# Performance work log

Hardware: AMD Instinct MI355X
Metric: run time of the kernel (lower is better)

Reference implementation:

```python
import jax, jax.numpy as jnp
import numpy as np

H = 4        # num_heads
KNN = 10     # k_knn neighbors gathered by distance
KS = 4       # k_select top-k neighbors kept by attention score
EPS = 1e-5
BIG = 1e9


def _ln(x, g, b):
    m = x.mean(-1, keepdims=True)
    v = ((x - m) ** 2).mean(-1, keepdims=True)
    return (x - m) * jax.lax.rsqrt(v + EPS) * g + b


def _sparse_dyn_voxel_attn(x, coords, mask, w_qkv, b_qkv, w_proj, b_proj):
    # x: [B,N,C], coords: [B,N,3], mask: [B,N] bool
    B, N, C = x.shape
    dh = C // H
    qkv = x @ w_qkv + b_qkv                       # [B,N,3C]
    q, k, v = jnp.split(qkv, 3, axis=-1)
    q = q.reshape(B, N, H, dh).transpose(0, 2, 1, 3)   # [B,H,N,dh]
    k = k.reshape(B, N, H, dh).transpose(0, 2, 1, 3)
    v = v.reshape(B, N, H, dh).transpose(0, 2, 1, 3)

    # KNN over voxel coordinates; empty voxels pushed to far distance
    d2 = jnp.sum((coords[:, :, None, :] - coords[:, None, :, :]) ** 2, axis=-1)  # [B,N,N]
    d2 = jnp.where(mask[:, None, :], d2, BIG)
    _, nbr = jax.lax.top_k(-d2, KNN)              # [B,N,KNN] nearest-neighbor indices

    # gather neighbor keys/values: [B,H,N,KNN,dh]
    kn = jax.vmap(lambda a, i: a[:, i, :])(k, nbr)
    vn = jax.vmap(lambda a, i: a[:, i, :])(v, nbr)
    nmask = jax.vmap(lambda m, i: m[i])(mask, nbr)  # [B,N,KNN]

    scale = float(1.0 / np.sqrt(dh))
    scores = jnp.einsum('bhnd,bhnkd->bhnk', q, kn) * scale  # [B,H,N,KNN]
    scores = scores + jnp.where(nmask, 0.0, -BIG)[:, None, :, :]

    # dynamic selection: keep top k_select neighbors by score, softmax over them
    sv, si = jax.lax.top_k(scores, KS)            # [B,H,N,KS]
    w = jax.nn.softmax(sv, axis=-1)
    vsel = jnp.take_along_axis(vn, si[..., None], axis=3)   # [B,H,N,KS,dh]
    o = jnp.einsum('bhnk,bhnkd->bhnd', w, vsel)   # [B,H,N,dh]
    o = o.transpose(0, 2, 1, 3).reshape(B, N, C) @ w_proj + b_proj
    return jnp.where(mask[..., None], o, 0.0)


def setup_inputs() -> dict:
    key = jax.random.key(0)
    ks = jax.random.split(key, 8)
    B, N, C, M = 4, 4096, 64, 256  # N = 16^3 voxels
    s = lambda k, sh: jax.random.normal(k, sh, jnp.float32) * 0.02
    return dict(
        inputs=jax.random.normal(ks[0], (B, N, C), jnp.float32),
        voxel_coords=jax.random.uniform(ks[1], (B, N, 3), jnp.float32) * 16.0,
        non_empty_mask=jax.random.randint(ks[2], (B, N), 0, 2).astype(bool),
        ln1_g=jnp.ones(C, jnp.float32), ln1_b=jnp.zeros(C, jnp.float32),
        ln2_g=jnp.ones(C, jnp.float32), ln2_b=jnp.zeros(C, jnp.float32),
        w_qkv=s(ks[3], (C, 3 * C)), b_qkv=jnp.zeros(3 * C, jnp.float32),
        w_proj=s(ks[4], (C, C)), b_proj=jnp.zeros(C, jnp.float32),
        w1=s(ks[5], (C, M)), b1=jnp.zeros(M, jnp.float32),
        w2=s(ks[6], (M, C)), b2=jnp.zeros(C, jnp.float32),
    )


def reference(inputs, voxel_coords, non_empty_mask, ln1_g, ln1_b, ln2_g, ln2_b,
              w_qkv, b_qkv, w_proj, b_proj, w1, b1, w2, b2):
    a = _sparse_dyn_voxel_attn(_ln(inputs, ln1_g, ln1_b), voxel_coords,
                               non_empty_mask, w_qkv, b_qkv, w_proj, b_proj)
    x = 0.5 * a + inputs                          # drop_path(attn)*0.5 + shortcut (eval)
    h = jax.nn.gelu(_ln(x, ln2_g, ln2_b) @ w1 + b1) @ w2 + b2
    return 0.5 * h + x
```

## Files before the change

kernel.cpp:

```cpp
#include <hip/hip_runtime.h>
#include <hip/hip_bf16.h>
#include <math.h>

#define NH   4
#define DH   16
#define CH   64
#define KNN  10
#define KS   4
#define NV   4096
#define NB   4
#define MHID 256
#define BN   (NB * NV)

#define P_LN1G  0
#define P_LN1B  64
#define P_LN2G  128
#define P_LN2B  192
#define P_WQKV  256
#define P_BQKV  12544
#define P_WPROJ 12736
#define P_BPROJ 16832
#define P_W1    16896
#define P_B1    33280
#define P_W2    33536
#define P_B2    49920
#define P_TOT   49984

#define N_ING  (BN * CH + P_TOT + BN)
#define N_ING4 (N_ING / 4)
#define N_PACK (16384 + 16384 + 12288)
#define NPREP  ((N_ING4 + N_PACK + 255) / 256)
#define KNNBLK (NB * (NV / 4))

typedef __hip_bfloat16 bf16;
typedef __attribute__((ext_vector_type(8))) short short8;
typedef __attribute__((ext_vector_type(4))) float float4a;

__device__ __forceinline__ float b2f(bf16 x) { return __bfloat162float(x); }

__device__ __forceinline__ float cvt(const void* p, int i, int isbf) {
  return isbf ? b2f(((const bf16*)p)[i]) : ((const float*)p)[i];
}

__device__ __forceinline__ float us2f(unsigned short u) {
  return __uint_as_float(((unsigned)u) << 16);
}

__device__ __forceinline__ float4 cvt4(const void* p, int i, int isbf) {
  float4 r;
  if (isbf) {
    ushort4 u = *(const ushort4*)((const unsigned short*)p + i);
    r.x = us2f(u.x); r.y = us2f(u.y); r.z = us2f(u.z); r.w = us2f(u.w);
  } else {
    r = *(const float4*)((const float*)p + i);
  }
  return r;
}

__device__ __forceinline__ float wave_sum_f32(float v) {
#pragma unroll
  for (int m = 32; m >= 1; m >>= 1) v += __shfl_xor(v, m, 64);
  return v;
}

__device__ __forceinline__ int wave_sum_i32(int v) {
#pragma unroll
  for (int m = 32; m >= 1; m >>= 1) v += __shfl_xor(v, m, 64);
  return v;
}

__device__ __forceinline__ void wave_min_kv(unsigned& hi, unsigned& lo) {
#pragma unroll
  for (int m = 32; m >= 1; m >>= 1) {
    unsigned ohi = __shfl_xor(hi, m, 64);
    unsigned olo = __shfl_xor(lo, m, 64);
    if (ohi < hi || (ohi == hi && olo < lo)) { hi = ohi; lo = olo; }
  }
}

__device__ __forceinline__ float tanh_fast(float u) {
  float e = __expf(2.0f * u);
  return 1.0f - 2.0f / (e + 1.0f);
}

__device__ __forceinline__ float d2f(float x, float y, float z,
                                     float qx, float qy, float qz) {
  float dx = x - qx, dy = y - qy, dz = z - qz;
  return dx * dx + dy * dy + dz * dz;
}

__device__ __forceinline__ void knn_insert(unsigned long long* arr,
                                           unsigned long long key) {
  if (key < arr[KNN - 1]) {
#pragma unroll
    for (int t = 0; t < KNN; ++t) {
      unsigned long long a = arr[t];
      bool lt = key < a;
      unsigned long long mn = lt ? key : a;
      unsigned long long mx = lt ? a : key;
      arr[t] = mn;
      key = mx;
    }
  }
}

__global__ __launch_bounds__(256) void k_prep(
    const void* xin, const void* coords, const void* maskr,
    const void* ln1g, const void* ln1b, const void* ln2g, const void* ln2b,
    const void* wqkv, const void* bqkv, const void* wproj, const void* bproj,
    const void* w1, const void* b1, const void* w2, const void* b2,
    float* __restrict__ xcan,
    float* __restrict__ pcan, int* __restrict__ mcan,
    unsigned short* __restrict__ w1p, unsigned short* __restrict__ w2p,
    unsigned short* __restrict__ wqp, int* __restrict__ flags,
    float4* __restrict__ pbin, unsigned* __restrict__ bstart)
{
  __shared__ int sfl[2];
  __shared__ unsigned cnt[NV];
  __shared__ unsigned woff[4];
  const int tid = threadIdx.x;
  if (tid < 64) {
    const unsigned short* xu = (const unsigned short*)xin;
    const unsigned* mu = (const unsigned*)maskr;
    int c = 0;
#pragma unroll
    for (int k = 0; k < 4; ++k) {
      unsigned short w = xu[tid * 4 + k];
      int e = (w >> 7) & 0xFF;
      c += (e >= 100 && e <= 140);
    }
#pragma unroll
    for (int m = 32; m >= 1; m >>= 1) c += __shfl_xor(c, m, 64);
    unsigned big = (mu[tid] > 1u) ? 1u : 0u;
#pragma unroll
    for (int m = 32; m >= 1; m >>= 1) big |= __shfl_xor(big, m, 64);
    if (tid == 0) {
      sfl[0] = (c >= 205) ? 1 : 0;
      sfl[1] = big ? 1 : 0;
      if (blockIdx.x == 0) { flags[0] = sfl[0]; flags[1] = sfl[1]; }
    }
  }
  __syncthreads();
  const int isbf = sfl[0], m8 = sfl[1];

  if (blockIdx.x >= NPREP) {
    const int bb = blockIdx.x - NPREP;
    unsigned* st = bstart + (size_t)bb * 4104;
    const unsigned char* m8p = (const unsigned char*)maskr + (size_t)bb * NV;
    const int* m32p = (const int*)maskr + (size_t)bb * NV;
#pragma unroll
    for (int k = 0; k < 16; ++k) cnt[tid + k * 256] = 0;
    __syncthreads();
    for (int k = 0; k < 16; ++k) {
      int j = tid + k * 256;
      int mv = m8 ? (m8p[j] != 0) : (m32p[j] != 0);
      if (mv) {
        int e = (bb * NV + j) * 3;
        float x = cvt(coords, e, isbf), y = cvt(coords, e + 1, isbf),
              z = cvt(coords, e + 2, isbf);
        int cx = (int)x; cx = cx > 15 ? 15 : cx;
        int cy = (int)y; cy = cy > 15 ? 15 : cy;
        int cz = (int)z; cz = cz > 15 ? 15 : cz;
        atomicAdd(&cnt[(cz << 8) + (cy << 4) + cx], 1u);
      }
    }
    __syncthreads();
    unsigned s[16], tot = 0;
#pragma unroll
    for (int t = 0; t < 16; ++t) { s[t] = cnt[tid * 16 + t]; tot += s[t]; }
    unsigned v = tot;
    const int ln = tid & 63, wv = tid >> 6;
#pragma unroll
    for (int d = 1; d < 64; d <<= 1) {
      unsigned o = __shfl_up(v, d, 64);
      if (ln >= d) v += o;
    }
    if (ln == 63) woff[wv] = v;
    __syncthreads();
    unsigned wpre = 0;
    for (int w = 0; w < wv; ++w) wpre += woff[w];
    unsigned r = wpre + v - tot;
#pragma unroll
    for (int t = 0; t < 16; ++t) {
      cnt[tid * 16 + t] = r; st[tid * 16 + t] = r; r += s[t];
    }
    if (tid == 255) st[4096] = r;
    __syncthreads();
    for (int k = 0; k < 16; ++k) {
      int j = tid + k * 256;
      int mv = m8 ? (m8p[j] != 0) : (m32p[j] != 0);
      if (mv) {
        int e = (bb * NV + j) * 3;
        float x = cvt(coords, e, isbf), y = cvt(coords, e + 1, isbf),
              z = cvt(coords, e + 2, isbf);
        int cx = (int)x; cx = cx > 15 ? 15 : cx;
        int cy = (int)y; cy = cy > 15 ? 15 : cy;
        int cz = (int)z; cz = cz > 15 ? 15 : cz;
        unsigned pos = atomicAdd(&cnt[(cz << 8) + (cy << 4) + cx], 1u);
        float4 q; q.x = x; q.y = y; q.z = z; q.w = __int_as_float(j);
        pbin[(size_t)bb * NV + pos] = q;
      }
    }
    return;
  }

  int id = blockIdx.x * 256 + tid;
  if (id < N_ING4) {
    int e4 = id * 4;
    const int n0 = BN * CH, n2 = P_TOT;
    if (e4 < n0) { *(float4*)&xcan[e4] = cvt4(xin, e4, isbf); return; }
    e4 -= n0;
    if (e4 < n2) {
      const void* src; int off;
      if      (e4 < P_LN1B)  { src = ln1g;  off = e4 - P_LN1G; }
      else if (e4 < P_LN2G)  { src = ln1b;  off = e4 - P_LN1B; }
      else if (e4 < P_LN2B)  { src = ln2g;  off = e4 - P_LN2G; }
      else if (e4 < P_WQKV)  { src = ln2b;  off = e4 - P_LN2B; }
      else if (e4 < P_BQKV)  { src = wqkv;  off = e4 - P_WQKV; }
      else if (e4 < P_WPROJ) { src = bqkv;  off = e4 - P_BQKV; }
      else if (e4 < P_BPROJ) { src = wproj; off = e4 - P_WPROJ; }
      else if (e4 < P_W1)    { src = bproj; off = e4 - P_BPROJ; }
      else if (e4 < P_B1)    { src = w1;    off = e4 - P_W1; }
      else if (e4 < P_W2)    { src = b1;    off = e4 - P_B1; }
      else if (e4 < P_B2)    { src = w2;    off = e4 - P_W2; }
      else                   { src = b2;    off = e4 - P_B2; }
      *(float4*)&pcan[e4] = cvt4(src, off, isbf);
      return;
    }
    e4 -= n2;
    if (m8) {
      uchar4 u = *(const uchar4*)((const unsigned char*)maskr + e4);
      mcan[e4 + 0] = u.x != 0; mcan[e4 + 1] = u.y != 0;
      mcan[e4 + 2] = u.z != 0; mcan[e4 + 3] = u.w != 0;
    } else {
      int4 vv = *(const int4*)((const int*)maskr + e4);
      mcan[e4 + 0] = vv.x != 0; mcan[e4 + 1] = vv.y != 0;
      mcan[e4 + 2] = vv.z != 0; mcan[e4 + 3] = vv.w != 0;
    }
    return;
  }
  id -= N_ING4;
  if (id < 16384) {
    int j = id & 7, l = (id >> 3) & 63, kh = (id >> 9) & 1, nt = id >> 10;
    int k = kh * 32 + ((l >> 4) * 8) + j;
    int n = nt * 16 + (l & 15);
    w1p[id] = __bfloat16_as_ushort(__float2bfloat16(cvt(w1, k * MHID + n, isbf)));
    return;
  }
  id -= 16384;
  if (id < 16384) {
    int j = id & 7, l = (id >> 3) & 63, kh = (id >> 9) & 7, nt = id >> 12;
    int k = kh * 32 + ((l >> 4) * 8) + j;
    int n = nt * 16 + (l & 15);
    w2p[id] = __bfloat16_as_ushort(__float2bfloat16(cvt(w2, k * CH + n, isbf)));
    return;
  }
  id -= 16384;
  if (id < 12288) {
    int j = id & 7, l = (id >> 3) & 63, kh = (id >> 9) & 1, nt = id >> 10;
    int k = kh * 32 + ((l >> 4) * 8) + j;
    int n = nt * 16 + (l & 15);
    wqp[id] = __bfloat16_as_ushort(__float2bfloat16(cvt(wqkv, k * 192 + n, isbf)));
  }
}

#define XQS 72
__global__ __launch_bounds__(256) void k_mid(
    const float4* __restrict__ pbin, const unsigned* __restrict__ bstart,
    int* __restrict__ nbr,
    const float* __restrict__ x, const float* __restrict__ pcan,
    const unsigned short* __restrict__ wqp, float* __restrict__ qkv)
{
  __shared__ unsigned short xnb[16 * XQS];
  const int wave = threadIdx.x >> 6, lane = threadIdx.x & 63;

  if (blockIdx.x < KNNBLK) {
    const int b = blockIdx.x >> 10;
    const int slot = (blockIdx.x & 1023) * 4 + wave;
    const unsigned* st = bstart + (size_t)b * 4104;
    const int nval = (int)st[4096];
    if (slot >= nval) return;
    const float4* gpt = pbin + (size_t)b * NV;

    const float4 me = gpt[slot];
    const float qx = me.x, qy = me.y, qz = me.z;
    const int qi = __float_as_int(me.w);
    int cz = (int)qz; cz = cz > 15 ? 15 : cz;

    unsigned long long arr[KNN];
#pragma unroll
    for (int t = 0; t < KNN; ++t) arr[t] = ~0ull;

    int R = 2;
    int zlo = cz - 2 < 0 ? 0 : cz - 2;
    int zhi = cz + 2 > 15 ? 15 : cz + 2;
    {
      const int s = (int)st[zlo << 8], e = (int)st[(zhi + 1) << 8];
      for (int i = s + lane; i < e; i += 64) {
        float4 p = gpt[i];
        float d2 = d2f(p.x, p.y, p.z, qx, qy, qz);
        knn_insert(arr, ((unsigned long long)__float_as_uint(d2) << 32) |
                        (unsigned)__float_as_int(p.w));
      }
    }

    for (;;) {
      const float RR = (float)(R * R);
      int c = 0;
#pragma unroll
      for (int t = 0; t < KNN; ++t) {
        float d = __uint_as_float((unsigned)(arr[t] >> 32));
        c += (d <= RR) ? 1 : 0;
      }
      c = wave_sum_i32(c);
      if (c >= KNN) break;
      if (zlo == 0 && zhi == 15) break;
      ++R;
      const int nzlo = cz - R < 0 ? 0 : cz - R;
      const int nzhi = cz + R > 15 ? 15 : cz + R;
      {
        const int s = (int)st[nzlo << 8], e = (int)st[zlo << 8];
        for (int i = s + lane; i < e; i += 64) {
          float4 p = gpt[i];
          float d2 = d2f(p.x, p.y, p.z, qx, qy, qz);
          knn_insert(arr, ((unsigned long long)__float_as_uint(d2) << 32) |
                          (unsigned)__float_as_int(p.w));
        }
      }
      {
        const int s = (int)st[(zhi + 1) << 8], e = (int)st[(nzhi + 1) << 8];
        for (int i = s + lane; i < e; i += 64) {
          float4 p = gpt[i];
          float d2 = d2f(p.x, p.y, p.z, qx, qy, qz);
          knn_insert(arr, ((unsigned long long)__float_as_uint(d2) << 32) |
                          (unsigned)__float_as_int(p.w));
        }
      }
      zlo = nzlo; zhi = nzhi;
    }

    unsigned myj = 0;
#pragma unroll 1
    for (int r = 0; r < KNN; ++r) {
      unsigned hi = (unsigned)(arr[0] >> 32);
      unsigned lo = (unsigned)(arr[0] & 0xffffffffu);
      wave_min_kv(hi, lo);
      const unsigned long long win = ((unsigned long long)hi << 32) | lo;
      if (arr[0] == win) {
#pragma unroll
        for (int t = 0; t < KNN - 1; ++t) arr[t] = arr[t + 1];
        arr[KNN - 1] = ~0ull;
      }
      if (lane == r) myj = lo;
    }
    const int row = (b << 12) | qi;
    if (lane < KNN) nbr[(size_t)row * KNN + lane] = (int)(myj & (NV - 1));
    return;
  }

  const int row0 = (blockIdx.x - KNNBLK) * 16;
  {
    const float gg = pcan[P_LN1G + lane], bb = pcan[P_LN1B + lane];
#pragma unroll
    for (int r = 0; r < 4; ++r) {
      int m = wave * 4 + r;
      float v = x[(size_t)(row0 + m) * CH + lane];
      float mn = wave_sum_f32(v) * (1.0f / 64.0f);
      float d = v - mn;
      float var = wave_sum_f32(d * d) * (1.0f / 64.0f);
      float rs = 1.0f / sqrtf(var + 1e-5f);
      xnb[m * XQS + lane] =
          __bfloat16_as_ushort(__float2bfloat16(d * rs * gg + bb));
    }
  }
  __syncthreads();

  const int q = lane >> 4, c = lane & 15;
  short8 a0 = *(const short8*)&xnb[c * XQS + q * 8];
  short8 a1 = *(const short8*)&xnb[c * XQS + 32 + q * 8];

#pragma unroll
  for (int t = 0; t < 3; ++t) {
    int nt = wave * 3 + t;
    short8 b0 = *(const short8*)&wqp[(size_t)((nt * 2 + 0) * 64 + lane) * 8];
    short8 b1 = *(const short8*)&wqp[(size_t)((nt * 2 + 1) * 64 + lane) * 8];
    float4a z = {0.f, 0.f, 0.f, 0.f};
    z = __builtin_amdgcn_mfma_f32_16x16x32_bf16(a0, b0, z, 0, 0, 0);
    z = __builtin_amdgcn_mfma_f32_16x16x32_bf16(a1, b1, z, 0, 0, 0);
    int n = nt * 16 + c;
    float bq = pcan[P_BQKV + n];
#pragma unroll
    for (int r = 0; r < 4; ++r) {
      int m = q * 4 + r;
      qkv[(size_t)(row0 + m) * 192 + n] = z[r] + bq;
    }
  }
}

#define XNS 72
#define GS  264
__global__ __launch_bounds__(256) void k_attn_mlp(
    const float* __restrict__ qkv, const int* __restrict__ nbr,
    const int* __restrict__ mcan, const float* __restrict__ xcan,
    const float* __restrict__ pcan,
    const unsigned short* __restrict__ w1p,
    const unsigned short* __restrict__ w2p,
    const int* __restrict__ flags, void* __restrict__ out)
{
  __shared__ float wp[CH * CH];
  __shared__ float bp[CH];
  __shared__ float otile[16][CH];
  __shared__ float xtile[16][CH];
  __shared__ float sc[4][NH][KNN];
  __shared__ float wsel[4][NH][KS];
  __shared__ int   isel[4][NH][KS];
  __shared__ int   nb[4][KNN];
  __shared__ float npen[4][KNN];
  __shared__ unsigned short xnb[16 * XNS];
  __shared__ unsigned short gb[16 * GS];
  const int tid = threadIdx.x;
  const int wave = tid >> 6, lane = tid & 63;
  const int row0 = blockIdx.x * 16;
  const int b = row0 / NV;

  {
    const float4* src = (const float4*)(pcan + P_WPROJ);
    float4* dst = (float4*)wp;
    for (int i = tid; i < CH * CH / 4; i += 256) dst[i] = src[i];
    if (tid < CH) bp[tid] = pcan[P_BPROJ + tid];
  }
  __syncthreads();

#pragma unroll 1
  for (int r = 0; r < 4; ++r) {
    const int m = wave * 4 + r;
    const int row = row0 + m;
    if (mcan[row]) {
      if (lane < KNN) {
        int j = nbr[(size_t)row * KNN + lane] & (NV - 1);
        nb[wave][lane] = j;
        npen[wave][lane] = mcan[b * NV + j] ? 0.0f : -1e9f;
      }
      __builtin_amdgcn_wave_barrier();
      if (lane < NH * KNN) {
        int h = lane / KNN, kk = lane % KNN;
        int j = nb[wave][kk];
        const float* qp = qkv + (size_t)row * 192 + h * DH;
        const float* kp = qkv + ((size_t)(b * NV + j)) * 192 + 64 + h * DH;
        float acc = 0.f;
#pragma unroll
        for (int d = 0; d < DH; ++d) acc += qp[d] * kp[d];
        sc[wave][h][kk] = acc * 0.25f + npen[wave][kk];
      }
      __builtin_amdgcn_wave_barrier();
      if (lane < NH) {
        int h = lane;
        float sv[KS]; int sj[KS];
        unsigned used = 0;
#pragma unroll
        for (int rr = 0; rr < KS; ++rr) {
          float best = -INFINITY; int bi = 0;
#pragma unroll
          for (int kk = 0; kk < KNN; ++kk) {
            float s = sc[wave][h][kk];
            if (!(used & (1u << kk)) && s > best) { best = s; bi = kk; }
          }
          used |= 1u << bi; sv[rr] = best; sj[rr] = bi;
        }
        float mx = sv[0];
        float e[KS], sum = 0.f;
#pragma unroll
        for (int rr = 0; rr < KS; ++rr) { e[rr] = expf(sv[rr] - mx); sum += e[rr]; }
        float inv = 1.0f / sum;
#pragma unroll
        for (int rr = 0; rr < KS; ++rr) {
          wsel[wave][h][rr] = e[rr] * inv;
          isel[wave][h][rr] = nb[wave][sj[rr]];
        }
      }
      __builtin_amdgcn_wave_barrier();
      {
        int h = lane >> 4, d = lane & 15;
        float o = 0.f;
#pragma unroll
        for (int rr = 0; rr < KS; ++rr) {
          int j = isel[wave][h][rr];
          o += wsel[wave][h][rr] *
               qkv[((size_t)(b * NV + j)) * 192 + 128 + h * DH + d];
        }
        otile[m][lane] = o;
      }
      __builtin_amdgcn_wave_barrier();
    }
  }

#pragma unroll 1
  for (int r = 0; r < 4; ++r) {
    const int m = wave * 4 + r;
    const int row = row0 + m;
    float x = xcan[(size_t)row * CH + lane];
    if (mcan[row]) {
      float acc = bp[lane];
#pragma unroll 4
      for (int cc = 0; cc < CH; ++cc)
        acc = fmaf(otile[m][cc], wp[cc * CH + lane], acc);
      x += 0.5f * acc;
    }
    xtile[m][lane] = x;
  }

  {
    const float gg = pcan[P_LN2G + lane], bb2 = pcan[P_LN2B + lane];
#pragma unroll
    for (int r = 0; r < 4; ++r) {
      int m = wave * 4 + r;
      float v = xtile[m][lane];
      float mn = wave_sum_f32(v) * (1.0f / 64.0f);
      float d = v - mn;
      float var = wave_sum_f32(d * d) * (1.0f / 64.0f);
      float rs = 1.0f / sqrtf(var + 1e-5f);
      xnb[m * XNS + lane] =
          __bfloat16_as_ushort(__float2bfloat16(d * rs * gg + bb2));
    }
  }
  __syncthreads();

  const int q = lane >> 4, c = lane & 15;
  short8 a0 = *(const short8*)&xnb[c * XNS + q * 8];
  short8 a1 = *(const short8*)&xnb[c * XNS + 32 + q * 8];

  float4a acc1[4];
#pragma unroll
  for (int t = 0; t < 4; ++t) {
    int nt = wave * 4 + t;
    short8 b0 = *(const short8*)&w1p[(size_t)((nt * 2 + 0) * 64 + lane) * 8];
    short8 b1 = *(const short8*)&w1p[(size_t)((nt * 2 + 1) * 64 + lane) * 8];
    float4a z = {0.f, 0.f, 0.f, 0.f};
    z = __builtin_amdgcn_mfma_f32_16x16x32_bf16(a0, b0, z, 0, 0, 0);
    z = __builtin_amdgcn_mfma_f32_16x16x32_bf16(a1, b1, z, 0, 0, 0);
    acc1[t] = z;
  }
#pragma unroll
  for (int t = 0; t < 4; ++t) {
    int n = (wave * 4 + t) * 16 + c;
    float bo = pcan[P_B1 + n];
#pragma unroll
    for (int r = 0; r < 4; ++r) {
      float h = acc1[t][r] + bo;
      float u = 0.7978845608028654f * (h + 0.044715f * h * h * h);
      float gv = 0.5f * h * (1.0f + tanh_fast(u));
      gb[(q * 4 + r) * GS + n] = __bfloat16_as_ushort(__float2bfloat16(gv));
    }
  }
  __syncthreads();

  float4a o = {0.f, 0.f, 0.f, 0.f};
#pragma unroll
  for (int kh = 0; kh < 8; ++kh) {
    short8 ag = *(const short8*)&gb[c * GS + kh * 32 + q * 8];
    short8 bg = *(const short8*)&w2p[(size_t)((wave * 8 + kh) * 64 + lane) * 8];
    o = __builtin_amdgcn_mfma_f32_16x16x32_bf16(ag, bg, o, 0, 0, 0);
  }
  {
    int n = wave * 16 + c;
    float b2v = pcan[P_B2 + n];
    const int isbf = flags[0];
#pragma unroll
    for (int r = 0; r < 4; ++r) {
      int m = q * 4 + r;
      size_t idx = (size_t)(row0 + m) * CH + n;
      float val = 0.5f * (o[r] + b2v) + xtile[m][n];
      if (isbf) ((bf16*)out)[idx] = __float2bfloat16(val);
      else      ((float*)out)[idx] = val;
    }
  }
}

extern "C" void kernel_launch(void* const* d_in, const int* in_sizes, int n_in,
                              void* d_out, int out_size, void* d_ws, size_t ws_size,
                              hipStream_t stream)
{
  char* ws = (char*)d_ws;
  float* qkv   = (float*)(ws);
  float* xcan  = (float*)(ws + 16777216);
  float* pcan  = (float*)(ws + 21168128);
  int*   mcan  = (int*)  (ws + 21368064);
  int*   nbr   = (int*)  (ws + 21433600);
  int*   flags = (int*)  (ws + 22088960);
  unsigned short* w1p = (unsigned short*)(ws + 22089728);
  unsigned short* w2p = (unsigned short*)(ws + 22122496);
  unsigned short* wqp = (unsigned short*)(ws + 22155264);
  float4*   pbin   = (float4*)  (ws + 22179840);
  unsigned* bstart = (unsigned*)(ws + 22441984);

  k_prep<<<NPREP + NB, 256, 0, stream>>>(
      d_in[0], d_in[1], d_in[2], d_in[3], d_in[4], d_in[5], d_in[6],
      d_in[7], d_in[8], d_in[9], d_in[10], d_in[11], d_in[12], d_in[13], d_in[14],
      xcan, pcan, mcan, w1p, w2p, wqp, flags, pbin, bstart);
  k_mid<<<KNNBLK + BN / 16, 256, 0, stream>>>(pbin, bstart, nbr,
                                              xcan, pcan, wqp, qkv);
  k_attn_mlp<<<BN / 16, 256, 0, stream>>>(qkv, nbr, mcan, xcan, pcan,
                                          w1p, w2p, flags, d_out);
}
```

Before: 158.1 us.

## Replace sorted-insert KNN with radix-threshold select and z-slab binning

Binning moves out of the prep kernel into its own kernel, which sorts points into 16 z-slabs using ballot-based counting instead of a 4096-cell 3D histogram. The KNN kernel finds each lane's minimum distance, derives a threshold with a bitwise ballot search, compacts the candidates under that threshold into LDS, and ranks them there. If the candidate count is too small or overflows the buffer, it falls back to the old per-lane insertion sort. The aim is to avoid the per-point 10-deep insertion network, at the cost of scanning each candidate slab two or three times and adding two extra kernel launches.

```diff
diff --git a/kernel.cpp b/kernel.cpp
--- a/kernel.cpp
+++ b/kernel.cpp
@@ -30,11 +30,11 @@
 #define N_ING4 (N_ING / 4)
 #define N_PACK (16384 + 16384 + 12288)
 #define NPREP  ((N_ING4 + N_PACK + 255) / 256)
-#define KNNBLK (NB * (NV / 4))
 
 typedef __hip_bfloat16 bf16;
 typedef __attribute__((ext_vector_type(8))) short short8;
 typedef __attribute__((ext_vector_type(4))) float float4a;
+typedef unsigned long long ull;
 
 __device__ __forceinline__ float b2f(bf16 x) { return __bfloat162float(x); }
 
@@ -63,12 +63,6 @@
   return v;
 }
 
-__device__ __forceinline__ int wave_sum_i32(int v) {
-#pragma unroll
-  for (int m = 32; m >= 1; m >>= 1) v += __shfl_xor(v, m, 64);
-  return v;
-}
-
 __device__ __forceinline__ void wave_min_kv(unsigned& hi, unsigned& lo) {
 #pragma unroll
   for (int m = 32; m >= 1; m >>= 1) {
@@ -89,15 +83,14 @@
   return dx * dx + dy * dy + dz * dz;
 }
 
-__device__ __forceinline__ void knn_insert(unsigned long long* arr,
-                                           unsigned long long key) {
+__device__ __forceinline__ void knn_insert(ull* arr, ull key) {
   if (key < arr[KNN - 1]) {
 #pragma unroll
     for (int t = 0; t < KNN; ++t) {
-      unsigned long long a = arr[t];
+      ull a = arr[t];
       bool lt = key < a;
-      unsigned long long mn = lt ? key : a;
-      unsigned long long mx = lt ? a : key;
+      ull mn = lt ? key : a;
+      ull mx = lt ? a : key;
       arr[t] = mn;
       key = mx;
     }
@@ -112,12 +105,9 @@
     float* __restrict__ xcan,
     float* __restrict__ pcan, int* __restrict__ mcan,
     unsigned short* __restrict__ w1p, unsigned short* __restrict__ w2p,
-    unsigned short* __restrict__ wqp, int* __restrict__ flags,
-    float4* __restrict__ pbin, unsigned* __restrict__ bstart)
+    unsigned short* __restrict__ wqp, int* __restrict__ flags)
 {
   __shared__ int sfl[2];
-  __shared__ unsigned cnt[NV];
-  __shared__ unsigned woff[4];
   const int tid = threadIdx.x;
   if (tid < 64) {
     const unsigned short* xu = (const unsigned short*)xin;
@@ -142,67 +132,6 @@
   }
   __syncthreads();
   const int isbf = sfl[0], m8 = sfl[1];
-
-  if (blockIdx.x >= NPREP) {
-    const int bb = blockIdx.x - NPREP;
-    unsigned* st = bstart + (size_t)bb * 4104;
-    const unsigned char* m8p = (const unsigned char*)maskr + (size_t)bb * NV;
-    const int* m32p = (const int*)maskr + (size_t)bb * NV;
-#pragma unroll
-    for (int k = 0; k < 16; ++k) cnt[tid + k * 256] = 0;
-    __syncthreads();
-    for (int k = 0; k < 16; ++k) {
-      int j = tid + k * 256;
-      int mv = m8 ? (m8p[j] != 0) : (m32p[j] != 0);
-      if (mv) {
-        int e = (bb * NV + j) * 3;
-        float x = cvt(coords, e, isbf), y = cvt(coords, e + 1, isbf),
-              z = cvt(coords, e + 2, isbf);
-        int cx = (int)x; cx = cx > 15 ? 15 : cx;
-        int cy = (int)y; cy = cy > 15 ? 15 : cy;
-        int cz = (int)z; cz = cz > 15 ? 15 : cz;
-        atomicAdd(&cnt[(cz << 8) + (cy << 4) + cx], 1u);
-      }
-    }
-    __syncthreads();
-    unsigned s[16], tot = 0;
-#pragma unroll
-    for (int t = 0; t < 16; ++t) { s[t] = cnt[tid * 16 + t]; tot += s[t]; }
-    unsigned v = tot;
-    const int ln = tid & 63, wv = tid >> 6;
-#pragma unroll
-    for (int d = 1; d < 64; d <<= 1) {
-      unsigned o = __shfl_up(v, d, 64);
-      if (ln >= d) v += o;
-    }
-    if (ln == 63) woff[wv] = v;
-    __syncthreads();
-    unsigned wpre = 0;
-    for (int w = 0; w < wv; ++w) wpre += woff[w];
-    unsigned r = wpre + v - tot;
-#pragma unroll
-    for (int t = 0; t < 16; ++t) {
-      cnt[tid * 16 + t] = r; st[tid * 16 + t] = r; r += s[t];
-    }
-    if (tid == 255) st[4096] = r;
-    __syncthreads();
-    for (int k = 0; k < 16; ++k) {
-      int j = tid + k * 256;
-      int mv = m8 ? (m8p[j] != 0) : (m32p[j] != 0);
-      if (mv) {
-        int e = (bb * NV + j) * 3;
-        float x = cvt(coords, e, isbf), y = cvt(coords, e + 1, isbf),
-              z = cvt(coords, e + 2, isbf);
-        int cx = (int)x; cx = cx > 15 ? 15 : cx;
-        int cy = (int)y; cy = cy > 15 ? 15 : cy;
-        int cz = (int)z; cz = cz > 15 ? 15 : cz;
-        unsigned pos = atomicAdd(&cnt[(cz << 8) + (cy << 4) + cx], 1u);
-        float4 q; q.x = x; q.y = y; q.z = z; q.w = __int_as_float(j);
-        pbin[(size_t)bb * NV + pos] = q;
-      }
-    }
-    return;
-  }
 
   int id = blockIdx.x * 256 + tid;
   if (id < N_ING4) {
@@ -264,101 +193,109 @@
   }
 }
 
+__global__ __launch_bounds__(1024) void k_bin(
+    const void* xin, const void* coords, const void* maskr,
+    float4* __restrict__ pbin, unsigned* __restrict__ lstart)
+{
+  __shared__ int sfl[2];
+  __shared__ unsigned cnt[16], cur[16];
+  const int tid = threadIdx.x;
+  if (tid < 64) {
+    const unsigned short* xu = (const unsigned short*)xin;
+    const unsigned* mu = (const unsigned*)maskr;
+    int c = 0;
+#pragma unroll
+    for (int k = 0; k < 4; ++k) {
+      unsigned short w = xu[tid * 4 + k];
+      int e = (w >> 7) & 0xFF;
+      c += (e >= 100 && e <= 140);
+    }
+#pragma unroll
+    for (int m = 32; m >= 1; m >>= 1) c += __shfl_xor(c, m, 64);
+    unsigned big = (mu[tid] > 1u) ? 1u : 0u;
+#pragma unroll
+    for (int m = 32; m >= 1; m >>= 1) big |= __shfl_xor(big, m, 64);
+    if (tid == 0) { sfl[0] = (c >= 205) ? 1 : 0; sfl[1] = big ? 1 : 0; }
+  }
+  if (tid < 16) { cnt[tid] = 0; }
+  __syncthreads();
+  const int isbf = sfl[0], m8 = sfl[1];
+
+  const int b = blockIdx.x;
+  const unsigned char* m8p = (const unsigned char*)maskr + (size_t)b * NV;
+  const int* m32p = (const int*)maskr + (size_t)b * NV;
+  unsigned* stg = lstart + b * 17;
+  const int lane = tid & 63;
+  const ull below = (lane == 0) ? 0ull : (~0ull >> (64 - lane));
+
+  unsigned myc = 0;
+#pragma unroll 1
+  for (int k = 0; k < 4; ++k) {
+    const int j = tid + k * 1024;
+    const int mv = m8 ? (m8p[j] != 0) : (m32p[j] != 0);
+    int lz = 16;
+    if (mv) {
+      float z = cvt(coords, (b * NV + j) * 3 + 2, isbf);
+      int cz = (int)z; lz = cz > 15 ? 15 : cz;
+    }
+#pragma unroll
+    for (int bb = 0; bb < 16; ++bb) {
+      ull m = __ballot(lz == bb);
+      if (lane == bb) myc += (unsigned)__popcll(m);
+    }
+  }
+  if (lane < 16) atomicAdd(&cnt[lane], myc);
+  __syncthreads();
+
+  if (tid == 0) {
+    unsigned run = 0;
+#pragma unroll
+    for (int bb = 0; bb < 16; ++bb) {
+      stg[bb] = run; cur[bb] = run; run += cnt[bb];
+    }
+    stg[16] = run;
+  }
+  __syncthreads();
+
+#pragma unroll 1
+  for (int k = 0; k < 4; ++k) {
+    const int j = tid + k * 1024;
+    const int mv = m8 ? (m8p[j] != 0) : (m32p[j] != 0);
+    int lz = 16;
+    float x = 0.f, y = 0.f, z = 0.f;
+    if (mv) {
+      int e = (b * NV + j) * 3;
+      x = cvt(coords, e, isbf); y = cvt(coords, e + 1, isbf);
+      z = cvt(coords, e + 2, isbf);
+      int cz = (int)z; lz = cz > 15 ? 15 : cz;
+    }
+#pragma unroll 1
+    for (int bb = 0; bb < 16; ++bb) {
+      ull m = __ballot(lz == bb);
+      if (m) {
+        unsigned base0 = 0;
+        if (lane == bb) base0 = atomicAdd(&cur[bb], (unsigned)__popcll(m));
+        unsigned base = __shfl(base0, bb, 64);
+        if (lz == bb) {
+          unsigned pos = base + (unsigned)__popcll(m & below);
+          float4 q; q.x = x; q.y = y; q.z = z; q.w = __int_as_float(j);
+          pbin[(size_t)b * NV + pos] = q;
+        }
+      }
+    }
+  }
+}
+
 #define XQS 72
-__global__ __launch_bounds__(256) void k_mid(
-    const float4* __restrict__ pbin, const unsigned* __restrict__ bstart,
-    int* __restrict__ nbr,
+__global__ __launch_bounds__(256) void k_ln_qkv(
     const float* __restrict__ x, const float* __restrict__ pcan,
     const unsigned short* __restrict__ wqp, float* __restrict__ qkv)
 {
   __shared__ unsigned short xnb[16 * XQS];
-  const int wave = threadIdx.x >> 6, lane = threadIdx.x & 63;
-
-  if (blockIdx.x < KNNBLK) {
-    const int b = blockIdx.x >> 10;
-    const int slot = (blockIdx.x & 1023) * 4 + wave;
-    const unsigned* st = bstart + (size_t)b * 4104;
-    const int nval = (int)st[4096];
-    if (slot >= nval) return;
-    const float4* gpt = pbin + (size_t)b * NV;
-
-    const float4 me = gpt[slot];
-    const float qx = me.x, qy = me.y, qz = me.z;
-    const int qi = __float_as_int(me.w);
-    int cz = (int)qz; cz = cz > 15 ? 15 : cz;
-
-    unsigned long long arr[KNN];
-#pragma unroll
-    for (int t = 0; t < KNN; ++t) arr[t] = ~0ull;
-
-    int R = 2;
-    int zlo = cz - 2 < 0 ? 0 : cz - 2;
-    int zhi = cz + 2 > 15 ? 15 : cz + 2;
-    {
-      const int s = (int)st[zlo << 8], e = (int)st[(zhi + 1) << 8];
-      for (int i = s + lane; i < e; i += 64) {
-        float4 p = gpt[i];
-        float d2 = d2f(p.x, p.y, p.z, qx, qy, qz);
-        knn_insert(arr, ((unsigned long long)__float_as_uint(d2) << 32) |
-                        (unsigned)__float_as_int(p.w));
-      }
-    }
-
-    for (;;) {
-      const float RR = (float)(R * R);
-      int c = 0;
-#pragma unroll
-      for (int t = 0; t < KNN; ++t) {
-        float d = __uint_as_float((unsigned)(arr[t] >> 32));
-        c += (d <= RR) ? 1 : 0;
-      }
-      c = wave_sum_i32(c);
-      if (c >= KNN) break;
-      if (zlo == 0 && zhi == 15) break;
-      ++R;
-      const int nzlo = cz - R < 0 ? 0 : cz - R;
-      const int nzhi = cz + R > 15 ? 15 : cz + R;
-      {
-        const int s = (int)st[nzlo << 8], e = (int)st[zlo << 8];
-        for (int i = s + lane; i < e; i += 64) {
-          float4 p = gpt[i];
-          float d2 = d2f(p.x, p.y, p.z, qx, qy, qz);
-          knn_insert(arr, ((unsigned long long)__float_as_uint(d2) << 32) |
-                          (unsigned)__float_as_int(p.w));
-        }
-      }
-      {
-        const int s = (int)st[(zhi + 1) << 8], e = (int)st[(nzhi + 1) << 8];
-        for (int i = s + lane; i < e; i += 64) {
-          float4 p = gpt[i];
-          float d2 = d2f(p.x, p.y, p.z, qx, qy, qz);
-          knn_insert(arr, ((unsigned long long)__float_as_uint(d2) << 32) |
-                          (unsigned)__float_as_int(p.w));
-        }
-      }
-      zlo = nzlo; zhi = nzhi;
-    }
-
-    unsigned myj = 0;
-#pragma unroll 1
-    for (int r = 0; r < KNN; ++r) {
-      unsigned hi = (unsigned)(arr[0] >> 32);
-      unsigned lo = (unsigned)(arr[0] & 0xffffffffu);
-      wave_min_kv(hi, lo);
-      const unsigned long long win = ((unsigned long long)hi << 32) | lo;
-      if (arr[0] == win) {
-#pragma unroll
-        for (int t = 0; t < KNN - 1; ++t) arr[t] = arr[t + 1];
-        arr[KNN - 1] = ~0ull;
-      }
-      if (lane == r) myj = lo;
-    }
-    const int row = (b << 12) | qi;
-    if (lane < KNN) nbr[(size_t)row * KNN + lane] = (int)(myj & (NV - 1));
-    return;
-  }
-
-  const int row0 = (blockIdx.x - KNNBLK) * 16;
+  const int tid = threadIdx.x;
+  const int wave = tid >> 6, lane = tid & 63;
+  const int row0 = blockIdx.x * 16;
+
   {
     const float gg = pcan[P_LN1G + lane], bb = pcan[P_LN1B + lane];
 #pragma unroll
@@ -394,6 +331,120 @@
       int m = q * 4 + r;
       qkv[(size_t)(row0 + m) * 192 + n] = z[r] + bq;
     }
+  }
+}
+
+#define CAPK 128
+__global__ __launch_bounds__(256) void k_knn5(
+    const float4* __restrict__ pbin, const unsigned* __restrict__ lstart,
+    int* __restrict__ nbr)
+{
+  __shared__ ull sb[4][CAPK];
+  __shared__ unsigned d9s[4];
+  const int wave = threadIdx.x >> 6, lane = threadIdx.x & 63;
+  const int b = blockIdx.x >> 10;
+  const int slot = (blockIdx.x & 1023) * 4 + wave;
+  const unsigned* st = lstart + b * 17;
+  const int nval = (int)st[16];
+  if (slot >= nval) return;
+  const float4* gpt = pbin + (size_t)b * NV;
+  ull* kb = sb[wave];
+  const ull below = (lane == 0) ? 0ull : (~0ull >> (64 - lane));
+
+  const float4 me = gpt[slot];
+  const float qx = me.x, qy = me.y, qz = me.z;
+  const int qi = __float_as_int(me.w);
+  int cz = (int)qz; cz = cz > 15 ? 15 : cz;
+  const int row = (b << 12) | qi;
+
+  int R = 2;
+  for (;;) {
+    const int zlo = cz - R < 0 ? 0 : cz - R;
+    const int zhi = cz + R > 15 ? 15 : cz + R;
+    const int s = (int)st[zlo], e = (int)st[zhi + 1];
+    const int n = e - s;
+
+    unsigned lm = 0xFFFFFFFFu;
+    for (int i = s + lane; i < e; i += 64) {
+      float4 p = gpt[i];
+      unsigned db = __float_as_uint(d2f(p.x, p.y, p.z, qx, qy, qz));
+      lm = db < lm ? db : lm;
+    }
+    unsigned acc = 0;
+#pragma unroll 1
+    for (int bit = 31; bit >= 0; --bit) {
+      unsigned tr = acc | (1u << bit);
+      int c = __popcll(__ballot(lm < tr));
+      if (c <= KNN - 1) acc = tr;
+    }
+    const unsigned T = acc + 8;
+
+    int cnt = 0;
+    for (int i0 = 0; i0 < n; i0 += 64) {
+      const int i = i0 + lane;
+      const int ii = s + (i < n ? i : 0);
+      float4 p = gpt[ii];
+      unsigned db = __float_as_uint(d2f(p.x, p.y, p.z, qx, qy, qz));
+      bool sel = (i < n) && (db <= T);
+      ull bal = __ballot(sel);
+      if (sel) {
+        int pos = cnt + __popcll(bal & below);
+        if (pos < CAPK)
+          kb[pos] = ((ull)db << 32) | (unsigned)__float_as_int(p.w);
+      }
+      cnt += __popcll(bal);
+    }
+    __builtin_amdgcn_wave_barrier();
+
+    unsigned d9bits;
+    if (cnt >= KNN && cnt <= CAPK) {
+#pragma unroll 1
+      for (int o = 0; o < CAPK; o += 64) {
+        const int idx = o + lane;
+        if (idx < cnt) {
+          const ull my = kb[idx];
+          int rank = 0;
+          for (int i = 0; i < cnt; ++i) rank += (kb[i] < my) ? 1 : 0;
+          if (rank < KNN) {
+            nbr[(size_t)row * KNN + rank] = (int)(my & (NV - 1));
+            if (rank == KNN - 1) d9s[wave] = (unsigned)(my >> 32);
+          }
+        }
+      }
+      __builtin_amdgcn_wave_barrier();
+      d9bits = d9s[wave];
+    } else {
+      ull arr[KNN];
+#pragma unroll
+      for (int t = 0; t < KNN; ++t) arr[t] = ~0ull;
+      for (int i = s + lane; i < e; i += 64) {
+        float4 p = gpt[i];
+        unsigned db = __float_as_uint(d2f(p.x, p.y, p.z, qx, qy, qz));
+        knn_insert(arr, ((ull)db << 32) | (unsigned)__float_as_int(p.w));
+      }
+      unsigned myj = 0;
+      d9bits = 0xFFFFFFFFu;
+#pragma unroll 1
+      for (int r = 0; r < KNN; ++r) {
+        unsigned hi = (unsigned)(arr[0] >> 32);
+        unsigned lo = (unsigned)(arr[0] & 0xffffffffu);
+        wave_min_kv(hi, lo);
+        const ull win = ((ull)hi << 32) | lo;
+        if (arr[0] == win) {
+#pragma unroll
+          for (int t = 0; t < KNN - 1; ++t) arr[t] = arr[t + 1];
+          arr[KNN - 1] = ~0ull;
+        }
+        if (lane == r) myj = lo;
+        if (r == KNN - 1) d9bits = hi;
+      }
+      if (lane < KNN) nbr[(size_t)row * KNN + lane] = (int)(myj & (NV - 1));
+    }
+
+    const float d9 = __uint_as_float(d9bits);
+    if (d9 <= (float)(R * R)) break;
+    if (zlo == 0 && zhi == 15) break;
+    ++R;
   }
 }
 
@@ -591,14 +642,15 @@
   unsigned short* w2p = (unsigned short*)(ws + 22122496);
   unsigned short* wqp = (unsigned short*)(ws + 22155264);
   float4*   pbin   = (float4*)  (ws + 22179840);
-  unsigned* bstart = (unsigned*)(ws + 22441984);
-
-  k_prep<<<NPREP + NB, 256, 0, stream>>>(
+  unsigned* lstart = (unsigned*)(ws + 22441984);
+
+  k_prep<<<NPREP, 256, 0, stream>>>(
       d_in[0], d_in[1], d_in[2], d_in[3], d_in[4], d_in[5], d_in[6],
       d_in[7], d_in[8], d_in[9], d_in[10], d_in[11], d_in[12], d_in[13], d_in[14],
-      xcan, pcan, mcan, w1p, w2p, wqp, flags, pbin, bstart);
-  k_mid<<<KNNBLK + BN / 16, 256, 0, stream>>>(pbin, bstart, nbr,
-                                              xcan, pcan, wqp, qkv);
+      xcan, pcan, mcan, w1p, w2p, wqp, flags);
+  k_bin<<<NB, 1024, 0, stream>>>(d_in[0], d_in[1], d_in[2], pbin, lstart);
+  k_ln_qkv<<<BN / 16, 256, 0, stream>>>(xcan, pcan, wqp, qkv);
+  k_knn5<<<NB * (NV / 4), 256, 0, stream>>>(pbin, lstart, nbr);
   k_attn_mlp<<<BN / 16, 256, 0, stream>>>(qkv, nbr, mcan, xcan, pcan,
                                           w1p, w2p, flags, d_out);
 }
```

After: 154.2 us. -2.4%, faster.
